# Kernel tuning notes

Measured on AMD Instinct MI355X. Metric: run time of the kernel, lower is better.

The kernel has to match this reference:

```python
import jax, jax.numpy as jnp
import numpy as np

DIM = 1024
HEADS = 16
DIM_HEAD = 64
DIM_INNER = HEADS * DIM_HEAD
R_MAJOR = 2.0
R_MINOR = 1.0
EPS = 1e-10
ATTN_SCALE = DIM_HEAD ** 0.5  # torch SDPA `scale` is a multiplier on q@k^T
S_QK_FACTOR = float(DIM)      # Scale forward multiplier: init / scale = 1.0 / (1/dim)


def toroidal_norm(t, axis=-1, R=R_MAJOR, r=R_MINOR, eps=EPS):
    """Project onto sphere, scale first half of `axis` by R, second by r, renormalize."""
    axis = axis % t.ndim
    n = jnp.linalg.norm(t, axis=axis, keepdims=True)
    sp = t / jnp.clip(n, eps)
    d = t.shape[axis]
    h = d // 2
    scale = jnp.concatenate([jnp.full((h,), R, t.dtype), jnp.full((d - h,), r, t.dtype)])
    bshape = [1] * t.ndim
    bshape[axis] = d
    tp = sp * scale.reshape(bshape)
    n2 = jnp.linalg.norm(tp, axis=axis, keepdims=True)
    return tp / jnp.clip(n2, eps)


def setup_inputs() -> dict:
    key = jax.random.key(0)
    ks = jax.random.split(key, 5)
    b, n = 4, 1024
    x = jax.random.normal(ks[0], (b, n, DIM), jnp.float32)
    std = DIM ** -0.5
    w_q = jax.random.normal(ks[1], (DIM_INNER, DIM), jnp.float32) * std
    w_k = jax.random.normal(ks[2], (DIM_INNER, DIM), jnp.float32) * std
    w_v = jax.random.normal(ks[3], (DIM_INNER, DIM), jnp.float32) * std
    w_o = jax.random.normal(ks[4], (DIM, DIM_INNER), jnp.float32) * std
    qk_scale_param = jnp.full((DIM_INNER,), 1.0 / DIM, jnp.float32)  # Scale init
    return {"x": x, "w_q": w_q, "w_k": w_k, "w_v": w_v, "w_o": w_o,
            "qk_scale_param": qk_scale_param}


def reference(x, w_q, w_k, w_v, w_o, qk_scale_param):
    b, n, _ = x.shape
    # parametrized (toroidal-normed) projection weights
    wq = toroidal_norm(w_q, axis=-1)
    wk = toroidal_norm(w_k, axis=-1)
    wv = toroidal_norm(w_v, axis=-1)
    wo = toroidal_norm(w_o, axis=0)  # norm_dim_in=False -> dim=0

    q = jnp.einsum('bnd,ed->bne', x, wq).reshape(b, n, HEADS, DIM_HEAD).transpose(0, 2, 1, 3)
    k = jnp.einsum('bnd,ed->bne', x, wk).reshape(b, n, HEADS, DIM_HEAD).transpose(0, 2, 1, 3)
    v = jnp.einsum('bnd,ed->bne', x, wv).reshape(b, n, HEADS, DIM_HEAD).transpose(0, 2, 1, 3)

    # toroidal norm over head dim
    q = toroidal_norm(q, axis=-1)
    k = toroidal_norm(k, axis=-1)

    # learned per-channel qk scale: param * (init / scale)
    s = (qk_scale_param * S_QK_FACTOR).reshape(HEADS, 1, DIM_HEAD)
    q = q * s

    scores = jnp.einsum('bhnd,bhmd->bhnm', q, k) * ATTN_SCALE
    causal = jnp.tril(jnp.ones((n, n), bool))
    scores = jnp.where(causal, scores, jnp.finfo(scores.dtype).min)
    attn = jax.nn.softmax(scores, axis=-1)
    out = jnp.einsum('bhnm,bhmd->bhnd', attn, v)  # b h n d

    out = out.transpose(0, 2, 1, 3).reshape(b, n, DIM_INNER)
    return jnp.einsum('bne,de->bnd', out, wo)
```

## Files before the change

### kernel.cpp

```cpp
#include <hip/hip_runtime.h>
#include <hip/hip_bf16.h>

#define HEADS 16
#define DH    64
#define BATCH 4
#define SEQ   1024
#define DIMD  1024
#define TOK   4096

typedef __attribute__((ext_vector_type(8))) short bf16x8;
typedef __attribute__((ext_vector_type(4))) float f32x4;
typedef __attribute__((ext_vector_type(16))) float f32x16;

typedef const void __attribute__((address_space(1)))* gas1_t;
typedef void __attribute__((address_space(3)))* las3_t;

#define GLOAD16(g,l) __builtin_amdgcn_global_load_lds((gas1_t)(g),(las3_t)(l),16,0,0)
#define MFMA_BF16(a,b,c) __builtin_amdgcn_mfma_f32_16x16x32_bf16((a),(b),(c),0,0,0)
#define MFMA32(a,b,c) __builtin_amdgcn_mfma_f32_32x32x16_bf16((a),(b),(c),0,0,0)
#define ZERO16 {0.f,0.f,0.f,0.f,0.f,0.f,0.f,0.f,0.f,0.f,0.f,0.f,0.f,0.f,0.f,0.f}

__device__ __forceinline__ ushort f2bf(float f){
  __hip_bfloat16 h = __float2bfloat16(f);
  return *reinterpret_cast<ushort*>(&h);
}
__device__ __forceinline__ uint packbf2(float a, float b){
  return (uint)f2bf(a) | ((uint)f2bf(b) << 16);
}
__device__ __forceinline__ uint xswap32(uint x){
  return (uint)__shfl_xor((int)x, 32);
}

__global__ __launch_bounds__(256) void prep_kernel(
    const float* __restrict__ x,
    const float* __restrict__ wq, const float* __restrict__ wk, const float* __restrict__ wv,
    const float* __restrict__ wo,
    ushort* __restrict__ xb,
    ushort* __restrict__ oq, ushort* __restrict__ ok, ushort* __restrict__ ov,
    ushort* __restrict__ wob, float* __restrict__ part)
{
  __shared__ float sp[4];
  int bid = blockIdx.x, t = threadIdx.x;
  if (bid < 2048){
    int i = bid*256 + t;
    const float4* x4 = (const float4*)x;
    float4 a = x4[2*i], b = x4[2*i+1];
    union { ushort s[8]; uint4 u; } uu;
    uu.s[0]=f2bf(a.x); uu.s[1]=f2bf(a.y); uu.s[2]=f2bf(a.z); uu.s[3]=f2bf(a.w);
    uu.s[4]=f2bf(b.x); uu.s[5]=f2bf(b.y); uu.s[6]=f2bf(b.z); uu.s[7]=f2bf(b.w);
    ((uint4*)xb)[i] = uu.u;
  } else if (bid < 5120){
    int bb = bid - 2048;
    int row = bb & 1023;
    int m = bb >> 10;
    const float* src = (m==0)?wq:((m==1)?wk:wv);
    ushort* dst = (m==0)?oq:((m==1)?ok:ov);
    float4 v = ((const float4*)(src + (size_t)row*1024))[t];
    float sc = (t<128)?2.f:1.f;
    float ss = sc*sc*(v.x*v.x + v.y*v.y + v.z*v.z + v.w*v.w);
    #pragma unroll
    for (int off=1; off<64; off<<=1) ss += __shfl_xor(ss, off);
    int w = t>>6, lane = t&63;
    if (lane==0) sp[w]=ss;
    __syncthreads();
    float tot = sp[0]+sp[1]+sp[2]+sp[3];
    float inv = rsqrtf(fmaxf(tot,1e-20f)) * sc;
    union { ushort s[4]; uint2 u; } o;
    o.s[0]=f2bf(v.x*inv); o.s[1]=f2bf(v.y*inv); o.s[2]=f2bf(v.z*inv); o.s[3]=f2bf(v.w*inv);
    ((uint2*)(dst + (size_t)row*1024))[t] = o.u;
  } else if (bid < 5632){
    int i = (bid-5120)*256 + t;
    float sc = ((i>>7) < 512) ? 2.f : 1.f;
    const float4* x4 = (const float4*)wo;
    float4 a = x4[2*i], b = x4[2*i+1];
    union { ushort s[8]; uint4 u; } uu;
    uu.s[0]=f2bf(a.x*sc); uu.s[1]=f2bf(a.y*sc); uu.s[2]=f2bf(a.z*sc); uu.s[3]=f2bf(a.w*sc);
    uu.s[4]=f2bf(b.x*sc); uu.s[5]=f2bf(b.y*sc); uu.s[6]=f2bf(b.z*sc); uu.s[7]=f2bf(b.w*sc);
    ((uint4*)wob)[i] = uu.u;
  } else {
    int rb = bid - 5632;
    float4 a = {0.f,0.f,0.f,0.f};
    #pragma unroll 4
    for (int r=0;r<32;r++){
      int row = rb*32+r;
      float4 v = ((const float4*)wo)[row*256 + t];
      float s2 = (row<512)?4.f:1.f;
      a.x += s2*v.x*v.x; a.y += s2*v.y*v.y; a.z += s2*v.z*v.z; a.w += s2*v.w*v.w;
    }
    ((float4*)part)[rb*256 + t] = a;
  }
}

__global__ __launch_bounds__(256) void wo_csum_kernel(const float* __restrict__ part,
                                                      float* __restrict__ colsum){
  int c = blockIdx.x*256 + threadIdx.x;
  float s = 0.f;
  #pragma unroll
  for (int j=0;j<32;j++) s += part[j*1024 + c];
  colsum[c] = s;
}

template<int NZ>
__global__ __launch_bounds__(256, 2) void gemm_fused_kernel(
    const ushort* __restrict__ A,
    const ushort* __restrict__ B0, const ushort* __restrict__ B1, const ushort* __restrict__ B2,
    void* dst0, void* dst1, void* dst2,
    const float* __restrict__ qparam, const float* __restrict__ colsum, int K)
{
  __shared__ ushort As[64*32];
  __shared__ ushort Bs[NZ*128*32];
  const int bm = blockIdx.x*64, bn = blockIdx.y*128;
  const int tid = threadIdx.x, lane = tid&63, w = tid>>6;
  const int wr = w>>1, wc = w&1;
  const int l15 = lane&15, l4 = lane>>4;
  const int row16 = lane&15, ch = lane>>4;

  const f32x4 zero4 = {0.f,0.f,0.f,0.f};
  f32x4 acc[NZ][2][4];
  #pragma unroll
  for (int z=0;z<NZ;z++)
    #pragma unroll
    for (int m=0;m<2;m++)
      #pragma unroll
      for (int n=0;n<4;n++) acc[z][m][n] = zero4;

  for (int k0=0; k0<K; k0+=32){
    __syncthreads();
    GLOAD16(A + (size_t)(bm + w*16 + row16)*K + k0 + ch*8, &As[w*512]);
    #pragma unroll
    for (int j=0;j<NZ*2;j++){
      int seg = j*4 + w;
      int z = seg>>3, s = seg&7;
      const ushort* Bp = (z==0)?B0:((z==1)?B1:B2);
      GLOAD16(Bp + (size_t)(bn + s*16 + row16)*K + k0 + ch*8, &Bs[seg*512]);
    }
    __syncthreads();
    bf16x8 af[2];
    #pragma unroll
    for (int m=0;m<2;m++)
      af[m] = *(const bf16x8*)&As[(wr*2+m)*512 + l4*128 + l15*8];
    #pragma unroll
    for (int z=0;z<NZ;z++){
      bf16x8 bfr[4];
      #pragma unroll
      for (int n=0;n<4;n++)
        bfr[n] = *(const bf16x8*)&Bs[z*4096 + (wc*4+n)*512 + l4*128 + l15*8];
      #pragma unroll
      for (int m=0;m<2;m++)
        #pragma unroll
        for (int n=0;n<4;n++)
          acc[z][m][n] = MFMA_BF16(af[m], bfr[n], acc[z][m][n]);
    }
  }

  if (NZ==3){
    #pragma unroll
    for (int z=0;z<3;z++){
      ushort* dst = (ushort*)((z==0)?dst0:((z==1)?dst1:dst2));
      float qs[4];
      #pragma unroll
      for (int n=0;n<4;n++){
        int e = bn + wc*64 + n*16 + l15;
        if (z==0)      qs[n] = qparam[e]*8192.f*1.44269504088896f;
        else if (z==2) qs[n] = rsqrtf(fmaxf(colsum[e],1e-20f));
        else           qs[n] = 1.f;
      }
      #pragma unroll
      for (int m=0;m<2;m++){
        float ssq[4] = {0.f,0.f,0.f,0.f};
        if (z<2){
          #pragma unroll
          for (int reg=0;reg<4;reg++){
            float s=0.f;
            #pragma unroll
            for (int n=0;n<4;n++){
              float scl2 = (n<2)?4.f:1.f;
              float vv = acc[z][m][n][reg];
              s += scl2*vv*vv;
            }
            ssq[reg]=s;
          }
          #pragma unroll
          for (int d=1; d<16; d<<=1){
            #pragma unroll
            for (int reg=0;reg<4;reg++) ssq[reg] += __shfl_xor(ssq[reg], d);
          }
        }
        #pragma unroll
        for (int n=0;n<4;n++){
          float scl = (n<2)?2.f:1.f;
          #pragma unroll
          for (int reg=0;reg<4;reg++){
            float val = acc[z][m][n][reg];
            if (z<2) val = val*scl*rsqrtf(fmaxf(ssq[reg],1e-20f))*qs[n];
            else     val = val*qs[n];
            int row = bm + wr*32 + m*16 + l4*4 + reg;
            int col = bn + wc*64 + n*16 + l15;
            int b = row>>10, nn = row&1023, h = col>>6, d = col&63;
            if (z==2)
              dst[(((size_t)b*HEADS+h)*DH + d)*SEQ + nn] = f2bf(val);
            else
              dst[(((size_t)b*HEADS+h)*SEQ + nn)*DH + d] = f2bf(val);
          }
        }
      }
    }
  } else {
    float* outp = (float*)dst0;
    #pragma unroll
    for (int m=0;m<2;m++)
      #pragma unroll
      for (int n=0;n<4;n++)
        #pragma unroll
        for (int reg=0;reg<4;reg++){
          int row = bm + wr*32 + m*16 + l4*4 + reg;
          int col = bn + wc*64 + n*16 + l15;
          outp[(size_t)row*DIMD + col] = acc[0][m][n][reg];
        }
  }
}

template<int NS, bool MASK>
__device__ __forceinline__ void attn_iter(
    const ushort* __restrict__ Kp, const ushort* __restrict__ Vp,
    int kvb, const bf16x8 (&qf)[4], int l31, int l1,
    f32x16& o0, f32x16& o1, float& m_s, float& l_s)
{
  bf16x8 kfa[4], kfb[4];
  #pragma unroll
  for (int md=0; md<4; md++)
    kfa[md] = *(const bf16x8*)&Kp[(size_t)(kvb + l31)*DH + md*16 + l1*8];
  if (NS==2){
    #pragma unroll
    for (int md=0; md<4; md++)
      kfb[md] = *(const bf16x8*)&Kp[(size_t)(kvb + 32 + l31)*DH + md*16 + l1*8];
  }
  bf16x8 vf0[2*NS], vf1[2*NS];
  #pragma unroll
  for (int kc=0; kc<2*NS; kc++){
    vf0[kc] = *(const bf16x8*)&Vp[(size_t)l31*SEQ      + kvb + kc*16 + l1*8];
    vf1[kc] = *(const bf16x8*)&Vp[(size_t)(32+l31)*SEQ + kvb + kc*16 + l1*8];
  }

  f32x16 s0 = ZERO16, s1 = ZERO16;
  __builtin_amdgcn_s_setprio(1);
  #pragma unroll
  for (int md=0; md<4; md++) s0 = MFMA32(kfa[md], qf[md], s0);
  if (NS==2){
    #pragma unroll
    for (int md=0; md<4; md++) s1 = MFMA32(kfb[md], qf[md], s1);
  }
  __builtin_amdgcn_s_setprio(0);

  if (MASK){
    f32x16& sm = (NS==2) ? s1 : s0;
    #pragma unroll
    for (int r=0;r<16;r++){
      int kvl = (r&3) + 8*(r>>2) + 4*l1;
      if (kvl > l31) sm[r] = -3.0e38f;
    }
  }

  float mx = -3.0e38f;
  #pragma unroll
  for (int r=0;r<16;r++) mx = fmaxf(mx, s0[r]);
  if (NS==2){
    #pragma unroll
    for (int r=0;r<16;r++) mx = fmaxf(mx, s1[r]);
  }
  mx = fmaxf(mx, __shfl_xor(mx, 32));
  float mnew = fmaxf(m_s, mx);
  float alpha = __builtin_amdgcn_exp2f(m_s - mnew);
  m_s = mnew;
  float rs = 0.f;
  #pragma unroll
  for (int r=0;r<16;r++){ s0[r] = __builtin_amdgcn_exp2f(s0[r]-mnew); rs += s0[r]; }
  if (NS==2){
    #pragma unroll
    for (int r=0;r<16;r++){ s1[r] = __builtin_amdgcn_exp2f(s1[r]-mnew); rs += s1[r]; }
  }
  rs += __shfl_xor(rs, 32);
  l_s = l_s*alpha + rs;

  #pragma unroll
  for (int r=0;r<16;r++){ o0[r] *= alpha; o1[r] *= alpha; }

  uint ru[16];
  #pragma unroll
  for (int j=0;j<8;j++) ru[j] = packbf2(s0[2*j], s0[2*j+1]);
  if (NS==2){
    #pragma unroll
    for (int j=0;j<8;j++) ru[8+j] = packbf2(s1[2*j], s1[2*j+1]);
  }
  union U4 { uint u[4]; bf16x8 v; };
  U4 fr[2*NS];
  #pragma unroll
  for (int j=0;j<NS;j++){
    uint px[8];
    #pragma unroll
    for (int k=0;k<8;k++) px[k] = xswap32(ru[8*j+k]);
    fr[2*j].u[0]   = l1 ? px[2]      : ru[8*j+0];
    fr[2*j].u[1]   = l1 ? px[3]      : ru[8*j+1];
    fr[2*j].u[2]   = l1 ? ru[8*j+2]  : px[0];
    fr[2*j].u[3]   = l1 ? ru[8*j+3]  : px[1];
    fr[2*j+1].u[0] = l1 ? px[6]      : ru[8*j+4];
    fr[2*j+1].u[1] = l1 ? px[7]      : ru[8*j+5];
    fr[2*j+1].u[2] = l1 ? ru[8*j+6]  : px[4];
    fr[2*j+1].u[3] = l1 ? ru[8*j+7]  : px[5];
  }

  __builtin_amdgcn_s_setprio(1);
  #pragma unroll
  for (int kc=0; kc<2*NS; kc++){
    o0 = MFMA32(vf0[kc], fr[kc].v, o0);
    o1 = MFMA32(vf1[kc], fr[kc].v, o1);
  }
  __builtin_amdgcn_s_setprio(0);
}

__device__ __forceinline__ void process_tile(
    int t, int par, int bh,
    const ushort* __restrict__ Q, const ushort* __restrict__ K,
    const ushort* __restrict__ VT, ushort* __restrict__ O,
    int l31, int l1)
{
  const size_t base  = (size_t)bh * SEQ * DH;
  const size_t vbase = (size_t)bh * DH * SEQ;
  const ushort* Kp = K + base;
  const ushort* Vp = VT + vbase;
  const int qbase = t*64 + par*32;

  bf16x8 qf[4];
  #pragma unroll
  for (int md=0; md<4; md++)
    qf[md] = *(const bf16x8*)&Q[base + (size_t)(qbase + l31)*DH + md*16 + l1*8];

  f32x16 o0 = ZERO16, o1 = ZERO16;
  float m_s = -3.0e38f, l_s = 0.f;

  for (int kt=0; kt<t; kt++)
    attn_iter<2,false>(Kp, Vp, kt*64, qf, l31, l1, o0, o1, m_s, l_s);
  if (par) attn_iter<2,true>(Kp, Vp, t*64, qf, l31, l1, o0, o1, m_s, l_s);
  else     attn_iter<1,true>(Kp, Vp, t*64, qf, l31, l1, o0, o1, m_s, l_s);

  float li = 1.0f / l_s;
  int b = bh >> 4, hh = bh & 15;
  int n = qbase + l31;
  ushort* orow = O + ((size_t)b*SEQ + n)*DIMD + hh*64;
  #pragma unroll
  for (int r=0;r<16;r++){
    int dl = (r&3) + 8*(r>>2) + 4*l1;
    orow[dl]    = f2bf(o0[r]*li);
    orow[32+dl] = f2bf(o1[r]*li);
  }
}

__global__ __launch_bounds__(256, 2) void attn_kernel(
    const ushort* __restrict__ Q, const ushort* __restrict__ K, const ushort* __restrict__ VT,
    ushort* __restrict__ O)
{
  int id = blockIdx.x;
  int p  = id >> 6;
  int r  = id & 63;
  int bh = (r&7)*8 + (r>>3);
  int tid = threadIdx.x, wi = tid>>6, lane = tid&63;
  int l31 = lane & 31, l1 = lane >> 5;
  int sel = (wi & 1) ^ (bh & 1);
  int t   = sel ? (15-p) : p;
  int par = wi >> 1;
  process_tile(t, par, bh, Q, K, VT, O, l31, l1);
}

extern "C" void kernel_launch(void* const* d_in, const int* in_sizes, int n_in,
                              void* d_out, int out_size, void* d_ws, size_t ws_size,
                              hipStream_t stream)
{
  const float* x      = (const float*)d_in[0];
  const float* w_q    = (const float*)d_in[1];
  const float* w_k    = (const float*)d_in[2];
  const float* w_v    = (const float*)d_in[3];
  const float* w_o    = (const float*)d_in[4];
  const float* qparam = (const float*)d_in[5];
  char* ws = (char*)d_ws;
  const size_t MB = 1u<<20;
  ushort* xb  = (ushort*)(ws);
  ushort* wqb = (ushort*)(ws + 8*MB);
  ushort* wkb = (ushort*)(ws + 10*MB);
  ushort* wvb = (ushort*)(ws + 12*MB);
  ushort* wob = (ushort*)(ws + 14*MB);
  ushort* qd  = (ushort*)(ws + 16*MB);
  ushort* kd  = (ushort*)(ws + 24*MB);
  ushort* vd  = (ushort*)(ws + 32*MB);
  ushort* att = xb;
  float* part = (float*)(ws + 40*MB);
  float* colsum = (float*)d_out + (out_size - 1024);

  prep_kernel<<<dim3(5664), dim3(256), 0, stream>>>(
      x, w_q, w_k, w_v, w_o, xb, wqb, wkb, wvb, wob, part);
  wo_csum_kernel<<<dim3(4), dim3(256), 0, stream>>>(part, colsum);
  gemm_fused_kernel<3><<<dim3(64,8), dim3(256), 0, stream>>>(
      xb, wqb, wkb, wvb, (void*)qd, (void*)kd, (void*)vd, qparam, colsum, DIMD);
  attn_kernel<<<dim3(512), dim3(256), 0, stream>>>(qd, kd, vd, att);
  gemm_fused_kernel<1><<<dim3(64,8), dim3(256), 0, stream>>>(
      att, wob, wob, wob, d_out, nullptr, nullptr, nullptr, nullptr, DIMD);
}
```

Baseline: 143.5 us.

## Replace LDS-staged GEMM with direct global-to-register MFMA loads split over grid z

The QKV and output GEMMs no longer stage tiles through shared memory with global_load_lds and barriers. Each wave now loads its A and B MFMA fragments straight from global memory into registers. The three projections are split across blockIdx.z instead of being fused into one block, and the QKV kernel uses a 128-row tile (MT=4) to get more A reuse per wave. This removes LDS traffic and __syncthreads, but gives up sharing of A across the Q/K/V projections and sharing of tiles between waves, and relies on L1/L2 caching for the strided 16-byte loads.

```diff
diff --git a/kernel.cpp b/kernel.cpp
--- a/kernel.cpp
+++ b/kernel.cpp
@@ -12,10 +12,6 @@
 typedef __attribute__((ext_vector_type(4))) float f32x4;
 typedef __attribute__((ext_vector_type(16))) float f32x16;
 
-typedef const void __attribute__((address_space(1)))* gas1_t;
-typedef void __attribute__((address_space(3)))* las3_t;
-
-#define GLOAD16(g,l) __builtin_amdgcn_global_load_lds((gas1_t)(g),(las3_t)(l),16,0,0)
 #define MFMA_BF16(a,b,c) __builtin_amdgcn_mfma_f32_16x16x32_bf16((a),(b),(c),0,0,0)
 #define MFMA32(a,b,c) __builtin_amdgcn_mfma_f32_32x32x16_bf16((a),(b),(c),0,0,0)
 #define ZERO16 {0.f,0.f,0.f,0.f,0.f,0.f,0.f,0.f,0.f,0.f,0.f,0.f,0.f,0.f,0.f,0.f}
@@ -100,122 +96,104 @@
   colsum[c] = s;
 }
 
-template<int NZ>
-__global__ __launch_bounds__(256, 2) void gemm_fused_kernel(
+template<int MODE, int MT>
+__global__ __launch_bounds__(256, 4) void gemm_direct_kernel(
     const ushort* __restrict__ A,
     const ushort* __restrict__ B0, const ushort* __restrict__ B1, const ushort* __restrict__ B2,
     void* dst0, void* dst1, void* dst2,
     const float* __restrict__ qparam, const float* __restrict__ colsum, int K)
 {
-  __shared__ ushort As[64*32];
-  __shared__ ushort Bs[NZ*128*32];
-  const int bm = blockIdx.x*64, bn = blockIdx.y*128;
+  const int z = blockIdx.z;
+  const ushort* Bp = (z==0)?B0:((z==1)?B1:B2);
+  const int bm = blockIdx.x*(MT*32), bn = blockIdx.y*128;
   const int tid = threadIdx.x, lane = tid&63, w = tid>>6;
   const int wr = w>>1, wc = w&1;
   const int l15 = lane&15, l4 = lane>>4;
-  const int row16 = lane&15, ch = lane>>4;
 
   const f32x4 zero4 = {0.f,0.f,0.f,0.f};
-  f32x4 acc[NZ][2][4];
-  #pragma unroll
-  for (int z=0;z<NZ;z++)
-    #pragma unroll
-    for (int m=0;m<2;m++)
-      #pragma unroll
-      for (int n=0;n<4;n++) acc[z][m][n] = zero4;
-
+  f32x4 acc[MT][4];
+  #pragma unroll
+  for (int m=0;m<MT;m++)
+    #pragma unroll
+    for (int n=0;n<4;n++) acc[m][n] = zero4;
+
+  const ushort* Ab = A  + (size_t)(bm + wr*(MT*16) + l15)*K + l4*8;
+  const ushort* Bb = Bp + (size_t)(bn + wc*64 + l15)*K + l4*8;
+
+  #pragma unroll 2
   for (int k0=0; k0<K; k0+=32){
-    __syncthreads();
-    GLOAD16(A + (size_t)(bm + w*16 + row16)*K + k0 + ch*8, &As[w*512]);
-    #pragma unroll
-    for (int j=0;j<NZ*2;j++){
-      int seg = j*4 + w;
-      int z = seg>>3, s = seg&7;
-      const ushort* Bp = (z==0)?B0:((z==1)?B1:B2);
-      GLOAD16(Bp + (size_t)(bn + s*16 + row16)*K + k0 + ch*8, &Bs[seg*512]);
-    }
-    __syncthreads();
-    bf16x8 af[2];
-    #pragma unroll
-    for (int m=0;m<2;m++)
-      af[m] = *(const bf16x8*)&As[(wr*2+m)*512 + l4*128 + l15*8];
-    #pragma unroll
-    for (int z=0;z<NZ;z++){
-      bf16x8 bfr[4];
+    bf16x8 af[MT], bfr[4];
+    #pragma unroll
+    for (int m=0;m<MT;m++) af[m]  = *(const bf16x8*)(Ab + (size_t)m*16*K + k0);
+    #pragma unroll
+    for (int n=0;n<4;n++)  bfr[n] = *(const bf16x8*)(Bb + (size_t)n*16*K + k0);
+    #pragma unroll
+    for (int m=0;m<MT;m++)
       #pragma unroll
       for (int n=0;n<4;n++)
-        bfr[n] = *(const bf16x8*)&Bs[z*4096 + (wc*4+n)*512 + l4*128 + l15*8];
-      #pragma unroll
-      for (int m=0;m<2;m++)
+        acc[m][n] = MFMA_BF16(af[m], bfr[n], acc[m][n]);
+  }
+
+  if (MODE==0){
+    ushort* dst = (ushort*)((z==0)?dst0:((z==1)?dst1:dst2));
+    float qs[4];
+    #pragma unroll
+    for (int n=0;n<4;n++){
+      int e = bn + wc*64 + n*16 + l15;
+      if (z==0)      qs[n] = qparam[e]*8192.f*1.44269504088896f;
+      else if (z==2) qs[n] = rsqrtf(fmaxf(colsum[e],1e-20f));
+      else           qs[n] = 1.f;
+    }
+    #pragma unroll
+    for (int m=0;m<MT;m++){
+      float ssq[4] = {0.f,0.f,0.f,0.f};
+      if (z<2){
         #pragma unroll
-        for (int n=0;n<4;n++)
-          acc[z][m][n] = MFMA_BF16(af[m], bfr[n], acc[z][m][n]);
-    }
-  }
-
-  if (NZ==3){
-    #pragma unroll
-    for (int z=0;z<3;z++){
-      ushort* dst = (ushort*)((z==0)?dst0:((z==1)?dst1:dst2));
-      float qs[4];
+        for (int reg=0;reg<4;reg++){
+          float s=0.f;
+          #pragma unroll
+          for (int n=0;n<4;n++){
+            float scl2 = (n<2)?4.f:1.f;
+            float vv = acc[m][n][reg];
+            s += scl2*vv*vv;
+          }
+          ssq[reg]=s;
+        }
+        #pragma unroll
+        for (int d=1; d<16; d<<=1){
+          #pragma unroll
+          for (int reg=0;reg<4;reg++) ssq[reg] += __shfl_xor(ssq[reg], d);
+        }
+      }
       #pragma unroll
       for (int n=0;n<4;n++){
-        int e = bn + wc*64 + n*16 + l15;
-        if (z==0)      qs[n] = qparam[e]*8192.f*1.44269504088896f;
-        else if (z==2) qs[n] = rsqrtf(fmaxf(colsum[e],1e-20f));
-        else           qs[n] = 1.f;
-      }
-      #pragma unroll
-      for (int m=0;m<2;m++){
-        float ssq[4] = {0.f,0.f,0.f,0.f};
-        if (z<2){
-          #pragma unroll
-          for (int reg=0;reg<4;reg++){
-            float s=0.f;
-            #pragma unroll
-            for (int n=0;n<4;n++){
-              float scl2 = (n<2)?4.f:1.f;
-              float vv = acc[z][m][n][reg];
-              s += scl2*vv*vv;
-            }
-            ssq[reg]=s;
-          }
-          #pragma unroll
-          for (int d=1; d<16; d<<=1){
-            #pragma unroll
-            for (int reg=0;reg<4;reg++) ssq[reg] += __shfl_xor(ssq[reg], d);
-          }
-        }
+        float scl = (n<2)?2.f:1.f;
         #pragma unroll
-        for (int n=0;n<4;n++){
-          float scl = (n<2)?2.f:1.f;
-          #pragma unroll
-          for (int reg=0;reg<4;reg++){
-            float val = acc[z][m][n][reg];
-            if (z<2) val = val*scl*rsqrtf(fmaxf(ssq[reg],1e-20f))*qs[n];
-            else     val = val*qs[n];
-            int row = bm + wr*32 + m*16 + l4*4 + reg;
-            int col = bn + wc*64 + n*16 + l15;
-            int b = row>>10, nn = row&1023, h = col>>6, d = col&63;
-            if (z==2)
-              dst[(((size_t)b*HEADS+h)*DH + d)*SEQ + nn] = f2bf(val);
-            else
-              dst[(((size_t)b*HEADS+h)*SEQ + nn)*DH + d] = f2bf(val);
-          }
+        for (int reg=0;reg<4;reg++){
+          float val = acc[m][n][reg];
+          if (z<2) val = val*scl*rsqrtf(fmaxf(ssq[reg],1e-20f))*qs[n];
+          else     val = val*qs[n];
+          int row = bm + wr*(MT*16) + m*16 + l4*4 + reg;
+          int col = bn + wc*64 + n*16 + l15;
+          int b = row>>10, nn = row&1023, h = col>>6, d = col&63;
+          if (z==2)
+            dst[(((size_t)b*HEADS+h)*DH + d)*SEQ + nn] = f2bf(val);
+          else
+            dst[(((size_t)b*HEADS+h)*SEQ + nn)*DH + d] = f2bf(val);
         }
       }
     }
   } else {
     float* outp = (float*)dst0;
     #pragma unroll
-    for (int m=0;m<2;m++)
+    for (int m=0;m<MT;m++)
       #pragma unroll
       for (int n=0;n<4;n++)
         #pragma unroll
         for (int reg=0;reg<4;reg++){
-          int row = bm + wr*32 + m*16 + l4*4 + reg;
+          int row = bm + wr*(MT*16) + m*16 + l4*4 + reg;
           int col = bn + wc*64 + n*16 + l15;
-          outp[(size_t)row*DIMD + col] = acc[0][m][n][reg];
+          outp[(size_t)row*DIMD + col] = acc[m][n][reg];
         }
   }
 }
@@ -398,9 +376,9 @@
   prep_kernel<<<dim3(5664), dim3(256), 0, stream>>>(
       x, w_q, w_k, w_v, w_o, xb, wqb, wkb, wvb, wob, part);
   wo_csum_kernel<<<dim3(4), dim3(256), 0, stream>>>(part, colsum);
-  gemm_fused_kernel<3><<<dim3(64,8), dim3(256), 0, stream>>>(
+  gemm_direct_kernel<0,4><<<dim3(32,8,3), dim3(256), 0, stream>>>(
       xb, wqb, wkb, wvb, (void*)qd, (void*)kd, (void*)vd, qparam, colsum, DIMD);
   attn_kernel<<<dim3(512), dim3(256), 0, stream>>>(qd, kd, vd, att);
-  gemm_fused_kernel<1><<<dim3(64,8), dim3(256), 0, stream>>>(
+  gemm_direct_kernel<1,2><<<dim3(64,8,1), dim3(256), 0, stream>>>(
       att, wob, wob, wob, d_out, nullptr, nullptr, nullptr, nullptr, DIMD);
 }
```

Result: slower. 201.1 us (+40.2%).
